# Kernel tuning notes

Measured on AMD Instinct MI355X. Metric: run time of the kernel, lower is better.

## Reference

```python
import jax, jax.numpy as jnp
import numpy as np

R, A, B = 32, 16, 65536  # rules, antecedents, samples


def setup_inputs() -> dict:
    key = jax.random.key(0)
    k1, k2, k3 = jax.random.split(key, 3)
    input_data = jax.random.normal(k1, (B, A), dtype=jnp.float32)
    # abs(normal) like the original init; shift/scale keeps sigmas >= 1 so the
    # product of A Gaussian memberships stays well above fp32 underflow.
    FRB_W = jnp.abs(jax.random.normal(k2, (2 * R * A,), dtype=jnp.float32)) * 0.5 + 1.0
    C = jnp.abs(jax.random.normal(k3, (R, A + 1), dtype=jnp.float32))
    return {"input_data": input_data, "FRB_W": FRB_W, "C": C}


def reference(input_data, FRB_W, C):
    Rn = C.shape[0]
    An = C.shape[1] - 1
    # Faithful to the original indexing: locat_num = A*i + k, Gauss1 mf uses
    # FRB_weights[locat_num : locat_num+2] = (sigma, center) (overlapping windows).
    idx = jnp.arange(Rn)[:, None] * An + jnp.arange(An)[None, :]  # [R, A]
    sigma = FRB_W[idx]          # [R, A]
    center = FRB_W[idx + 1]     # [R, A]
    # Gauss1mf(x, [sigma, c]) = exp(-0.5 * ((x - c) / sigma)^2)
    z = (input_data[:, None, :] - center[None]) / sigma[None]      # [B, R, A]
    u = jnp.exp(-0.5 * z * z)                                      # [B, R, A]
    UU = jnp.prod(u, axis=-1)                                      # [B, R] rule firing strengths
    # TSK first-order consequent: C[:,0] bias + C[:,1:] @ x
    C_help = input_data @ C[:, 1:].T + C[:, 0]                     # [B, R]
    # weighted average over rules
    return jnp.sum(UU * C_help, axis=-1) / jnp.sum(UU, axis=-1)    # [B]
```

## Files before the change

### kernel.cpp

```cpp
#include <hip/hip_runtime.h>

#define RR 32
#define AA 16
#define SPLIT 4
#define RPW (RR / SPLIT)
#define BLOCK 256
#define SPB 64


__global__ __launch_bounds__(512) void tsk_precompute(
    const float* __restrict__ W,
    const float* __restrict__ C,
    float* __restrict__ P)
{
    __shared__ float cpart[RR * AA];
    const float LOG2E = 1.4426950408889634f;
    int t = threadIdx.x;
    if (t < RR * AA) {
        int r = t >> 4, k = t & 15;
        float sig = W[t];
        float c   = W[t + 1];
        float inv2 = 1.0f / (sig * sig);
        P[r * 64 + k]      = -0.5f * inv2 * LOG2E;
        P[r * 64 + 16 + k] = c * inv2 * LOG2E;
        cpart[t]           = -0.5f * c * c * inv2 * LOG2E;
        P[r * 64 + 32 + k] = C[r * (AA + 1) + 1 + k];
    }
    __syncthreads();
    if (t < RR) {
        float s = 0.0f;
        #pragma unroll
        for (int k = 0; k < AA; ++k) s += cpart[t * AA + k];
        P[t * 64 + 49] = s;
        P[t * 64 + 48] = C[t * (AA + 1)];
    }
}

__global__ __launch_bounds__(BLOCK, 4) void tsk_main(
    const float* __restrict__ x,
    const float* __restrict__ P,
    float* __restrict__ out,
    int B)
{
    __shared__ float pnum[SPLIT][SPB];
    __shared__ float pden[SPLIT][SPB];

    const int lane = threadIdx.x & 63;
    const int wv = __builtin_amdgcn_readfirstlane(threadIdx.x >> 6);

    int s = blockIdx.x * SPB + lane;
    int sl = s < B ? s : B - 1;

    const float4* xr = (const float4*)(x + (size_t)sl * AA);
    float4 v0 = xr[0], v1 = xr[1], v2 = xr[2], v3 = xr[3];
    float xv[AA] = { v0.x, v0.y, v0.z, v0.w,
                     v1.x, v1.y, v1.z, v1.w,
                     v2.x, v2.y, v2.z, v2.w,
                     v3.x, v3.y, v3.z, v3.w };
    float x2[AA];
    #pragma unroll
    for (int k = 0; k < AA; ++k) x2[k] = xv[k] * xv[k];

    float num = 0.0f, den = 0.0f;
    const float* pw = P + wv * RPW * 64;
    #pragma unroll 2
    for (int r = 0; r < RPW; ++r) {
        const float* p = pw + r * 64;
        float ea = 0.0f, eb = 0.0f;
        float ch = p[48];
        #pragma unroll
        for (int k = 0; k < AA; ++k) {
            ea = fmaf(p[k],      x2[k], ea);
            eb = fmaf(p[16 + k], xv[k], eb);
            ch = fmaf(p[32 + k], xv[k], ch);
        }
        float w = __builtin_amdgcn_exp2f(ea + eb + p[49]);
        num = fmaf(w, ch, num);
        den += w;
    }

    pnum[wv][lane] = num;
    pden[wv][lane] = den;
    __syncthreads();

    if (threadIdx.x < SPB) {
        int t = threadIdx.x;
        float n = pnum[0][t] + pnum[1][t] + pnum[2][t] + pnum[3][t];
        float d = pden[0][t] + pden[1][t] + pden[2][t] + pden[3][t];
        int so = blockIdx.x * SPB + t;
        if (so < B) out[so] = n * __builtin_amdgcn_rcpf(d);
    }
}

extern "C" void kernel_launch(void* const* d_in, const int* in_sizes, int n_in,
                              void* d_out, int out_size, void* d_ws, size_t ws_size,
                              hipStream_t stream) {
    const float* x = (const float*)d_in[0];
    const float* W = (const float*)d_in[1];
    const float* C = (const float*)d_in[2];
    float* out = (float*)d_out;
    float* P = (float*)d_ws;
    int B = in_sizes[0] / AA;

    tsk_precompute<<<dim3(1), dim3(512), 0, stream>>>(W, C, P);
    tsk_main<<<dim3((B + SPB - 1) / SPB), dim3(BLOCK), 0, stream>>>(x, P, out, B);
}
```

Before: 63.35 us.

## Fuse parameter precompute into main kernel, computing Gaussian terms inline

Removes the separate single-block precompute kernel and its workspace, so the main kernel reads sigma/center and consequent weights directly from the raw inputs. Each thread now evaluates (x-c)^2/sigma^2 with a reciprocal per antecedent instead of two FMAs against precomputed coefficients. This saves a kernel launch and the serialization between the two kernels. In exchange it adds per-element rcp and subtract work and recomputes it redundantly in every thread, and it uses the approximate rcp instead of a precise divide.

```diff
diff --git a/kernel.cpp b/kernel.cpp
--- a/kernel.cpp
+++ b/kernel.cpp
@@ -7,38 +7,10 @@
 #define BLOCK 256
 #define SPB 64
 
-
-__global__ __launch_bounds__(512) void tsk_precompute(
+__global__ __launch_bounds__(BLOCK, 4) void tsk_fused(
+    const float* __restrict__ x,
     const float* __restrict__ W,
     const float* __restrict__ C,
-    float* __restrict__ P)
-{
-    __shared__ float cpart[RR * AA];
-    const float LOG2E = 1.4426950408889634f;
-    int t = threadIdx.x;
-    if (t < RR * AA) {
-        int r = t >> 4, k = t & 15;
-        float sig = W[t];
-        float c   = W[t + 1];
-        float inv2 = 1.0f / (sig * sig);
-        P[r * 64 + k]      = -0.5f * inv2 * LOG2E;
-        P[r * 64 + 16 + k] = c * inv2 * LOG2E;
-        cpart[t]           = -0.5f * c * c * inv2 * LOG2E;
-        P[r * 64 + 32 + k] = C[r * (AA + 1) + 1 + k];
-    }
-    __syncthreads();
-    if (t < RR) {
-        float s = 0.0f;
-        #pragma unroll
-        for (int k = 0; k < AA; ++k) s += cpart[t * AA + k];
-        P[t * 64 + 49] = s;
-        P[t * 64 + 48] = C[t * (AA + 1)];
-    }
-}
-
-__global__ __launch_bounds__(BLOCK, 4) void tsk_main(
-    const float* __restrict__ x,
-    const float* __restrict__ P,
     float* __restrict__ out,
     int B)
 {
@@ -57,24 +29,28 @@
                      v1.x, v1.y, v1.z, v1.w,
                      v2.x, v2.y, v2.z, v2.w,
                      v3.x, v3.y, v3.z, v3.w };
-    float x2[AA];
-    #pragma unroll
-    for (int k = 0; k < AA; ++k) x2[k] = xv[k] * xv[k];
 
+    const float NHL2E = -0.7213475204444817f;
     float num = 0.0f, den = 0.0f;
-    const float* pw = P + wv * RPW * 64;
+
     #pragma unroll 2
     for (int r = 0; r < RPW; ++r) {
-        const float* p = pw + r * 64;
-        float ea = 0.0f, eb = 0.0f;
-        float ch = p[48];
+        const int ru = wv * RPW + r;
+        const float* pw = W + AA * ru;
+        const float* pc = C + ru * (AA + 1);
+
+        float q  = 0.0f;
+        float ch = pc[0];
         #pragma unroll
         for (int k = 0; k < AA; ++k) {
-            ea = fmaf(p[k],      x2[k], ea);
-            eb = fmaf(p[16 + k], xv[k], eb);
-            ch = fmaf(p[32 + k], xv[k], ch);
+            float sig  = pw[k];
+            float cen  = pw[k + 1];
+            float inv2 = __builtin_amdgcn_rcpf(sig * sig);
+            float t    = xv[k] - cen;
+            q  = fmaf(t * t, inv2, q);
+            ch = fmaf(pc[k + 1], xv[k], ch);
         }
-        float w = __builtin_amdgcn_exp2f(ea + eb + p[49]);
+        float w = __builtin_amdgcn_exp2f(q * NHL2E);
         num = fmaf(w, ch, num);
         den += w;
     }
@@ -99,9 +75,7 @@
     const float* W = (const float*)d_in[1];
     const float* C = (const float*)d_in[2];
     float* out = (float*)d_out;
-    float* P = (float*)d_ws;
     int B = in_sizes[0] / AA;
 
-    tsk_precompute<<<dim3(1), dim3(512), 0, stream>>>(W, C, P);
-    tsk_main<<<dim3((B + SPB - 1) / SPB), dim3(BLOCK), 0, stream>>>(x, P, out, B);
+    tsk_fused<<<dim3((B + SPB - 1) / SPB), dim3(BLOCK), 0, stream>>>(x, W, C, out, B);
 }
```

Result: no change. 64.35 us (+1.6%).
